# Kernel optimization log

Hardware: AMD Instinct MI355X
Metric: run time of the kernel (lower is better)

Reference implementation:

```python
import jax, jax.numpy as jnp
import numpy as np

DMODEL = 1024
DK = 64
DHEAD = 16
DEPTH = DK * DHEAD
N, LQ, L = 4, 4096, 4096
FAC1 = 1.0 / np.sqrt(DK)  # relu kernel scale folded into omega, as in reset()
EPS = 1e-6


def setup_inputs() -> dict:
    key = jax.random.key(0)
    ks = jax.random.split(key, 10)
    x = jax.random.normal(ks[0], (N, LQ, DMODEL), jnp.float32)
    y = jax.random.normal(ks[1], (N, L, DMODEL), jnp.float32)
    s_in = 1.0 / np.sqrt(DMODEL)
    s_depth = 1.0 / np.sqrt(DEPTH)
    # Linear weights stored as (in, out) so application is x @ W + b
    WQ = jax.random.normal(ks[2], (DMODEL, DEPTH), jnp.float32) * s_in
    WK = jax.random.normal(ks[3], (DMODEL, DEPTH), jnp.float32) * s_in
    WV = jax.random.normal(ks[4], (DMODEL, DEPTH), jnp.float32) * s_in
    WO = jax.random.normal(ks[5], (DEPTH, DMODEL), jnp.float32) * s_depth
    bQ = jnp.zeros((DEPTH,), jnp.float32)
    bK = jnp.zeros((DEPTH,), jnp.float32)
    bV = jnp.zeros((DEPTH,), jnp.float32)
    bO = jnp.zeros((DMODEL,), jnp.float32)
    # orthogonal random-feature projection: QR of gaussian, scaled by sqrt(dk), then *fac1 (relu)
    g = np.random.default_rng(0).standard_normal((DK, DK)).astype(np.float32)
    qmat, _ = np.linalg.qr(g)
    omega = jnp.asarray(qmat * np.sqrt(DK) * FAC1, dtype=jnp.float32)
    return dict(x=x, y=y, WQ=WQ, bQ=bQ, WK=WK, bK=bK, WV=WV, bV=bV,
                WO=WO, bO=bO, omega=omega)


def reference(x, y, WQ, bQ, WK, bK, WV, bV, WO, bO, omega):
    n, lq, _ = x.shape
    l = y.shape[1]
    # project and split heads: (n, h, L, dk)
    q = (x @ WQ + bQ).reshape(n, lq, DHEAD, DK).transpose(0, 2, 1, 3)
    k = (y @ WK + bK).reshape(n, l, DHEAD, DK).transpose(0, 2, 1, 3)
    v = (y @ WV + bV).reshape(n, l, DHEAD, DK).transpose(0, 2, 1, 3)
    # relu random-feature map phi(x) = relu(x @ omega) + eps
    q = jax.nn.relu(q @ omega) + EPS
    k = jax.nn.relu(k @ omega) + EPS
    # linear attention: out = phi(q) @ (phi(k)^T @ v) / (phi(q) @ phi(k)^T @ 1)
    kv = jnp.einsum('nhld,nhle->nhde', k, v)          # (n, h, dk, dk)
    ksum = jnp.sum(k, axis=2)                          # (n, h, dk)
    d_inv = jnp.einsum('nhqd,nhd->nhq', q, ksum)[..., None]
    out = jnp.einsum('nhqd,nhde->nhqe', q, kv) / d_inv  # (n, h, Lq, dk)
    out = out.transpose(0, 2, 1, 3).reshape(n, lq, DEPTH)
    return out @ WO + bO
```

## Files before the change

### kernel.cpp

```cpp
#include <hip/hip_runtime.h>

#define EPSF 1e-6f

typedef _Float16 f16x8 __attribute__((ext_vector_type(8)));
typedef _Float16 f16x4 __attribute__((ext_vector_type(4)));
typedef float    f32x4 __attribute__((ext_vector_type(4)));

#define GLL16(gp, lp) __builtin_amdgcn_global_load_lds( \
    (const __attribute__((address_space(1))) void*)(gp), \
    (__attribute__((address_space(3))) void*)(lp), 16, 0, 0)

__global__ __launch_bounds__(256) void cvt_f16(const float* __restrict__ in,
                                               _Float16* __restrict__ out, int n8) {
    int idx = blockIdx.x * 256 + threadIdx.x;
    int stride = gridDim.x * 256;
    for (; idx < n8; idx += stride) {
        const float4* p = (const float4*)in + (size_t)idx * 2;
        float4 a = p[0], b = p[1];
        f16x8 o;
        o[0] = (_Float16)a.x; o[1] = (_Float16)a.y; o[2] = (_Float16)a.z; o[3] = (_Float16)a.w;
        o[4] = (_Float16)b.x; o[5] = (_Float16)b.y; o[6] = (_Float16)b.z; o[7] = (_Float16)b.w;
        *(f16x8*)(out + (size_t)idx * 8) = o;
    }
}

__global__ __launch_bounds__(256) void build_obdT(const float* __restrict__ omega,
                                                  _Float16* __restrict__ obdT) {
    int idx = blockIdx.x * 256 + threadIdx.x;
    int c = idx >> 10, k = idx & 1023;
    float v = ((c >> 6) == (k >> 6)) ? omega[(k & 63) * 64 + (c & 63)] : 0.f;
    obdT[idx] = (_Float16)v;
}

__global__ __launch_bounds__(256) void transpose_cvt(const float* __restrict__ in,
                                                     _Float16* __restrict__ out) {
    __shared__ float tile[64][65];
    const int t = threadIdx.x;
    const int k0 = blockIdx.x * 64, n0 = blockIdx.y * 64;
#pragma unroll
    for (int j = 0; j < 16; j++) {
        int idx = j * 256 + t; int r = idx >> 6, c = idx & 63;
        tile[r][c] = in[(size_t)(k0 + r) * 1024 + n0 + c];
    }
    __syncthreads();
#pragma unroll
    for (int j = 0; j < 16; j++) {
        int idx = j * 256 + t; int rn = idx >> 6, ck = idx & 63;
        out[(size_t)(n0 + rn) * 1024 + k0 + ck] = (_Float16)tile[ck][rn];
    }
}

__global__ __launch_bounds__(256) void prep_bias(const float* __restrict__ bQ,
                                                 const float* __restrict__ bK,
                                                 const float* __restrict__ bV,
                                                 const float* __restrict__ omega,
                                                 float* __restrict__ bQf,
                                                 float* __restrict__ bkv) {
    int c = blockIdx.x * 256 + threadIdx.x;
    int h = c >> 6, e = c & 63;
    float sq = 0.f, sk = 0.f;
    for (int d = 0; d < 64; d++) {
        float o = omega[d * 64 + e];
        sq += bQ[h * 64 + d] * o;
        sk += bK[h * 64 + d] * o;
    }
    bQf[c] = sq;
    bkv[c] = sk;
    bkv[1024 + c] = bV[c];
}

__global__ __launch_bounds__(256) void gemm_fold(const _Float16* __restrict__ A,
                                                 const _Float16* __restrict__ Bt,
                                                 _Float16* __restrict__ out0,
                                                 _Float16* __restrict__ out1) {
    const int K = 1024;
    __shared__ __align__(16) _Float16 Asm[128 * 32];
    __shared__ __align__(16) _Float16 Bsm[128 * 32];
    const int t = threadIdx.x, lane = t & 63, w = t >> 6;
    const int bm = blockIdx.y * 128, bn = blockIdx.x * 128;
    const int wm = (w >> 1) * 64, wn = (w & 1) * 64;
    const int r15 = lane & 15, slog = lane >> 4;

    int aoff[4], boff[4];
#pragma unroll
    for (int m = 0; m < 4; m++) {
        int ra = wm + m * 16 + r15;
        aoff[m] = ra * 32 + (slog ^ ((ra >> 1) & 3)) * 8;
        int rb = wn + m * 16 + r15;
        boff[m] = rb * 32 + (slog ^ ((rb >> 1) & 3)) * 8;
    }
    f32x4 acc[4][4];
#pragma unroll
    for (int m = 0; m < 4; m++)
#pragma unroll
        for (int n = 0; n < 4; n++) acc[m][n] = (f32x4){0.f, 0.f, 0.f, 0.f};

    for (int kt = 0; kt < K; kt += 32) {
        __syncthreads();
#pragma unroll
        for (int i = 0; i < 2; i++) {
            int seg = i * 256 + w * 64 + lane;
            int r = seg >> 2, sp = seg & 3;
            int sg = sp ^ ((r >> 1) & 3);
            GLL16(A  + (size_t)(bm + r) * K + kt + sg * 8, Asm + (size_t)(i * 256 + w * 64) * 8);
            GLL16(Bt + (size_t)(bn + r) * K + kt + sg * 8, Bsm + (size_t)(i * 256 + w * 64) * 8);
        }
        __syncthreads();
        f16x8 av[4], bv[4];
#pragma unroll
        for (int m = 0; m < 4; m++) av[m] = *(const f16x8*)(Asm + aoff[m]);
#pragma unroll
        for (int n = 0; n < 4; n++) bv[n] = *(const f16x8*)(Bsm + boff[n]);
#pragma unroll
        for (int m = 0; m < 4; m++)
#pragma unroll
            for (int n = 0; n < 4; n++)
                acc[m][n] = __builtin_amdgcn_mfma_f32_16x16x32_f16(av[m], bv[n], acc[m][n], 0, 0, 0);
    }

#pragma unroll
    for (int m = 0; m < 4; m++) {
        int row0 = bm + wm + m * 16 + slog * 4;
        _Float16* C = (row0 < 1024) ? out0 : out1;
        int l = row0 & 1023;
#pragma unroll
        for (int n = 0; n < 4; n++) {
            int colg = bn + wn + n * 16 + r15;
            f16x4 p;
#pragma unroll
            for (int j = 0; j < 4; j++) p[j] = (_Float16)acc[m][n][j];
            *(f16x4*)(C + (size_t)colg * 1024 + l) = p;
        }
    }
}

template<int EPI>
__global__ __launch_bounds__(512, 2) void gemm256(const _Float16* __restrict__ A,
                                                  const _Float16* __restrict__ Bt,
                                                  const float* __restrict__ bias,
                                                  void* __restrict__ out0,
                                                  void* __restrict__ out1,
                                                  int M, int N, int K, int nbn) {
    __shared__ __align__(16) char lds[131072];
    const int t = threadIdx.x, lane = t & 63, w = t >> 6;
    const int nwg = gridDim.x;
    const int f = (blockIdx.x & 7) * (nwg >> 3) + (blockIdx.x >> 3);
    const int bm = (f / nbn) * 256, bn = (f % nbn) * 256;
    const int wm = (w & 1) * 128, wn = (w >> 1) * 64;
    const int r15 = lane & 15, hi = lane >> 4;
    const int srow = lane >> 2, sp = lane & 3;

    int aoff[8], boff[4];
#pragma unroll
    for (int m = 0; m < 8; m++) {
        int r = wm + m * 16 + r15;
        aoff[m] = r * 64 + (((hi + (r >> 1)) & 3) << 4);
    }
#pragma unroll
    for (int n = 0; n < 4; n++) {
        int r = wn + n * 16 + r15;
        boff[n] = r * 64 + (((hi + (r >> 1)) & 3) << 4);
    }

    f32x4 acc[8][4];
#pragma unroll
    for (int m = 0; m < 8; m++)
#pragma unroll
        for (int n = 0; n < 4; n++) acc[m][n] = (f32x4){0.f, 0.f, 0.f, 0.f};

    auto stage = [&](int s) {
        char* base = lds + (s & 3) * 32768;
        int kt = s * 32;
#pragma unroll
        for (int p = 0; p < 2; p++) {
            int row = w * 32 + p * 16 + srow;
            int sg = (sp - ((row >> 1) & 3)) & 3;
            GLL16(A  + (size_t)(bm + row) * K + kt + sg * 8, base + w * 2048 + p * 1024);
            GLL16(Bt + (size_t)(bn + row) * K + kt + sg * 8, base + 16384 + w * 2048 + p * 1024);
        }
    };

    const int NS = K >> 5;
    stage(0); stage(1); stage(2);
    asm volatile("s_waitcnt vmcnt(8)" ::: "memory");
    asm volatile("s_barrier" ::: "memory");
    for (int s = 0; s < NS; ++s) {
        const char* La = lds + (s & 3) * 32768;
        const char* Lb = La + 16384;
        if (s + 3 < NS) stage(s + 3);
        f16x8 bv[4], avL[4];
#pragma unroll
        for (int n = 0; n < 4; n++) bv[n] = *(const f16x8*)(Lb + boff[n]);
#pragma unroll
        for (int m = 0; m < 4; m++) avL[m] = *(const f16x8*)(La + aoff[m]);
        asm volatile("s_barrier" ::: "memory");
        asm volatile("s_waitcnt lgkmcnt(0)" ::: "memory");
        __builtin_amdgcn_s_setprio(1);
#pragma unroll
        for (int m = 0; m < 4; m++)
#pragma unroll
            for (int n = 0; n < 4; n++)
                acc[m][n] = __builtin_amdgcn_mfma_f32_16x16x32_f16(avL[m], bv[n], acc[m][n], 0, 0, 0);
        __builtin_amdgcn_s_setprio(0);
        asm volatile("s_barrier" ::: "memory");
        f16x8 avH[4];
#pragma unroll
        for (int m = 0; m < 4; m++) avH[m] = *(const f16x8*)(La + aoff[m + 4]);
        if (s + 3 < NS)      asm volatile("s_waitcnt vmcnt(8)" ::: "memory");
        else if (s + 2 < NS) asm volatile("s_waitcnt vmcnt(4)" ::: "memory");
        else                 asm volatile("s_waitcnt vmcnt(0)" ::: "memory");
        asm volatile("s_barrier" ::: "memory");
        asm volatile("s_waitcnt lgkmcnt(0)" ::: "memory");
        __builtin_amdgcn_s_setprio(1);
#pragma unroll
        for (int m = 0; m < 4; m++)
#pragma unroll
            for (int n = 0; n < 4; n++)
                acc[m + 4][n] = __builtin_amdgcn_mfma_f32_16x16x32_f16(avH[m], bv[n], acc[m + 4][n], 0, 0, 0);
        __builtin_amdgcn_s_setprio(0);
        asm volatile("s_barrier" ::: "memory");
    }

    if (EPI == 3) {
        char* LW = lds + w * 16384;
        const int colg0 = bn + wn;
        const bool isK = colg0 < 1024;
        _Float16* Cb = isK ? (_Float16*)out0 : (_Float16*)out1;
        const int hd = (isK ? colg0 : colg0 - 1024) >> 6;
        const int nb = bm >> 12;
        const int l0 = (bm & 4095) + wm;
#pragma unroll
        for (int m = 0; m < 8; m++)
#pragma unroll
            for (int n = 0; n < 4; n++) {
                int d = n * 16 + r15;
                float bs = bias[colg0 + d];
                f16x4 pk;
#pragma unroll
                for (int j = 0; j < 4; j++) {
                    float xv = acc[m][n][j] + bs;
                    if (isK) xv = fmaxf(xv, 0.f) + EPSF;
                    pk[j] = (_Float16)xv;
                }
                *(f16x4*)(LW + d * 256 + ((m * 32 + hi * 8) ^ ((d & 15) << 4))) = pk;
            }
        _Float16* basep = Cb + (size_t)(nb * 16 + hd) * 64 * 4096 + l0;
#pragma unroll
        for (int pass = 0; pass < 16; pass++) {
            int d = pass * 4 + hi;
            f16x8 v = *(const f16x8*)(LW + d * 256 + ((r15 * 16) ^ ((d & 15) << 4)));
            *(f16x8*)(basep + (size_t)d * 4096 + r15 * 8) = v;
        }
    } else {
#pragma unroll
        for (int m = 0; m < 8; m++) {
            int row0 = bm + wm + m * 16 + hi * 4;
#pragma unroll
            for (int n = 0; n < 4; n++) {
                int colg = bn + wn + n * 16 + r15;
                float bs = bias ? bias[colg] : 0.f;
#pragma unroll
                for (int j = 0; j < 4; j++) {
                    float xv = acc[m][n][j] + bs;
                    if (EPI == 1) {
                        xv = fmaxf(xv, 0.f) + EPSF;
                        ((_Float16*)out0)[(size_t)(row0 + j) * N + colg] = (_Float16)xv;
                    } else {
                        ((float*)out0)[(size_t)(row0 + j) * N + colg] = xv;
                    }
                }
            }
        }
    }
}

__global__ __launch_bounds__(256) void ksum_kernel(const _Float16* __restrict__ KphiT,
                                                   float* __restrict__ ksum) {
    const int t = threadIdx.x, lane = t & 63, w = t >> 6;
    const int gid = blockIdx.x;
    const int head = gid >> 4;
    const int d = (gid & 15) * 4 + w;
    const _Float16* src = KphiT + ((size_t)head * 64 + d) * 4096;
    float s = 0.f;
#pragma unroll
    for (int i = 0; i < 8; i++) {
        f16x8 v = *(const f16x8*)(src + (size_t)(i * 64 + lane) * 8);
#pragma unroll
        for (int j = 0; j < 8; j++) s += (float)v[j];
    }
#pragma unroll
    for (int o = 32; o; o >>= 1) s += __shfl_xor(s, o, 64);
    if (lane == 0) ksum[(size_t)head * 64 + d] = s;
}

__global__ __launch_bounds__(256) void kvt_kernel(const _Float16* __restrict__ Vt,
                                                  const _Float16* __restrict__ KphiT,
                                                  float* __restrict__ kvpart) {
    const int t = threadIdx.x, lane = t & 63, w = t >> 6;
    const int head = blockIdx.y;
    const int l0 = blockIdx.x * 1024;
    __shared__ __align__(16) _Float16 As[64 * 128];
    __shared__ __align__(16) _Float16 Bs[64 * 128];
    const int r15 = lane & 15, slog = lane >> 4;
    f32x4 acc[4][4];
#pragma unroll
    for (int m = 0; m < 4; m++)
#pragma unroll
        for (int n = 0; n < 4; n++) acc[m][n] = (f32x4){0.f, 0.f, 0.f, 0.f};

    for (int it = 0; it < 8; it++) {
        __syncthreads();
        int lbase = l0 + it * 128;
#pragma unroll
        for (int i = 0; i < 4; i++) {
            int seg = i * 256 + w * 64 + lane;
            int r = seg >> 4, sp2 = seg & 15;
            int sg = sp2 ^ (r & 15);
            GLL16(Vt    + ((size_t)head * 64 + r) * 4096 + lbase + sg * 8, As + (size_t)(i * 256 + w * 64) * 8);
            GLL16(KphiT + ((size_t)head * 64 + r) * 4096 + lbase + sg * 8, Bs + (size_t)(i * 256 + w * 64) * 8);
        }
        __syncthreads();
        f16x8 av[4], bv[4];
#pragma unroll
        for (int m = 0; m < 4; m++) {
            int r = m * 16 + r15;
            int s2 = w * 4 + slog;
            int ph = s2 ^ (r & 15);
            av[m] = *(const f16x8*)(As + r * 128 + ph * 8);
            bv[m] = *(const f16x8*)(Bs + r * 128 + ph * 8);
        }
#pragma unroll
        for (int m = 0; m < 4; m++)
#pragma unroll
            for (int n = 0; n < 4; n++)
                acc[m][n] = __builtin_amdgcn_mfma_f32_16x16x32_f16(av[m], bv[n], acc[m][n], 0, 0, 0);
    }
    float* red = (float*)As;
    for (int ww = 0; ww < 4; ww++) {
        __syncthreads();
        if (w == ww) {
#pragma unroll
            for (int m = 0; m < 4; m++)
#pragma unroll
                for (int n = 0; n < 4; n++)
#pragma unroll
                    for (int j = 0; j < 4; j++) {
                        int row = m * 16 + slog * 4 + j, col = n * 16 + r15;
                        if (ww == 0) red[row * 64 + col] = acc[m][n][j];
                        else         red[row * 64 + col] += acc[m][n][j];
                    }
        }
    }
    __syncthreads();
    float* outp = kvpart + ((size_t)head * 4 + blockIdx.x) * 4096;
#pragma unroll
    for (int i = 0; i < 16; i++) { int idx = i * 256 + t; outp[idx] = red[idx]; }
}

__global__ __launch_bounds__(256) void numdiv_kernel(const _Float16* __restrict__ Qphi,
                                                     const float* __restrict__ kvpart,
                                                     const float* __restrict__ ksum,
                                                     _Float16* __restrict__ U) {
    const int t = threadIdx.x, lane = t & 63, w = t >> 6;
    const int h = blockIdx.y;
    const int m0 = blockIdx.x * 256;
    const int nb = m0 >> 12;
    const int head = nb * 16 + h;
    __shared__ __align__(16) _Float16 Qs[256 * 64];
    __shared__ __align__(16) _Float16 Bs[64 * 64];
    __shared__ float ksl[64];

#pragma unroll
    for (int i = 0; i < 8; i++) {
        int seg = i * 256 + w * 64 + lane;
        int r = seg >> 3, sp = seg & 7;
        int sg = sp ^ (r & 7);
        GLL16(Qphi + (size_t)(m0 + r) * 1024 + h * 64 + sg * 8, Qs + (size_t)(i * 256 + w * 64) * 8);
    }
#pragma unroll
    for (int i = 0; i < 2; i++) {
        int sidx = i * 256 + t;
        int r = sidx >> 3, p = sidx & 7;
        int sg = p ^ (r & 7);
        const float* s0 = kvpart + (size_t)head * 4 * 4096 + r * 64 + sg * 8;
        float4 v0 = {0.f, 0.f, 0.f, 0.f}, v1 = {0.f, 0.f, 0.f, 0.f};
#pragma unroll
        for (int c = 0; c < 4; c++) {
            float4 a = *(const float4*)(s0 + c * 4096);
            float4 b = *(const float4*)(s0 + c * 4096 + 4);
            v0.x += a.x; v0.y += a.y; v0.z += a.z; v0.w += a.w;
            v1.x += b.x; v1.y += b.y; v1.z += b.z; v1.w += b.w;
        }
        f16x8 o;
        o[0] = (_Float16)v0.x; o[1] = (_Float16)v0.y; o[2] = (_Float16)v0.z; o[3] = (_Float16)v0.w;
        o[4] = (_Float16)v1.x; o[5] = (_Float16)v1.y; o[6] = (_Float16)v1.z; o[7] = (_Float16)v1.w;
        *(f16x8*)(Bs + sidx * 8) = o;
    }
    if (t < 64) ksl[t] = ksum[(size_t)head * 64 + t];
    __syncthreads();

    const int r15 = lane & 15, slog = lane >> 4;
    f32x4 acc[4][4];
#pragma unroll
    for (int m = 0; m < 4; m++)
#pragma unroll
        for (int n = 0; n < 4; n++) acc[m][n] = (f32x4){0.f, 0.f, 0.f, 0.f};
    float dp[4] = {0.f, 0.f, 0.f, 0.f};

#pragma unroll
    for (int kk = 0; kk < 2; kk++) {
        float ks[8];
#pragma unroll
        for (int j = 0; j < 8; j++) ks[j] = ksl[kk * 32 + slog * 8 + j];
        f16x8 av[4], bv[4];
#pragma unroll
        for (int m = 0; m < 4; m++) {
            int r = w * 64 + m * 16 + r15;
            int ph = (kk * 4 + slog) ^ (r & 7);
            av[m] = *(const f16x8*)(Qs + r * 64 + ph * 8);
        }
#pragma unroll
        for (int n = 0; n < 4; n++) {
            int r = n * 16 + r15;
            int ph = (kk * 4 + slog) ^ (r & 7);
            bv[n] = *(const f16x8*)(Bs + r * 64 + ph * 8);
        }
#pragma unroll
        for (int m = 0; m < 4; m++)
#pragma unroll
            for (int j = 0; j < 8; j++) dp[m] += (float)av[m][j] * ks[j];
#pragma unroll
        for (int m = 0; m < 4; m++)
#pragma unroll
            for (int n = 0; n < 4; n++)
                acc[m][n] = __builtin_amdgcn_mfma_f32_16x16x32_f16(av[m], bv[n], acc[m][n], 0, 0, 0);
    }
#pragma unroll
    for (int m = 0; m < 4; m++) {
        dp[m] += __shfl_xor(dp[m], 16, 64);
        dp[m] += __shfl_xor(dp[m], 32, 64);
    }
#pragma unroll
    for (int m = 0; m < 4; m++) {
#pragma unroll
        for (int j = 0; j < 4; j++) {
            float den = __shfl(dp[m], slog * 4 + j, 64);
            float inv = __builtin_amdgcn_rcpf(den);
            int row = m0 + w * 64 + m * 16 + slog * 4 + j;
#pragma unroll
            for (int n = 0; n < 4; n++)
                U[(size_t)row * 1024 + h * 64 + n * 16 + r15] = (_Float16)(acc[m][n][j] * inv);
        }
    }
}

extern "C" void kernel_launch(void* const* d_in, const int* in_sizes, int n_in,
                              void* d_out, int out_size, void* d_ws, size_t ws_size,
                              hipStream_t stream) {
    (void)in_sizes; (void)n_in; (void)out_size; (void)ws_size;
    const float* x     = (const float*)d_in[0];
    const float* y     = (const float*)d_in[1];
    const float* WQ    = (const float*)d_in[2];
    const float* bQ    = (const float*)d_in[3];
    const float* WK    = (const float*)d_in[4];
    const float* bK    = (const float*)d_in[5];
    const float* WV    = (const float*)d_in[6];
    const float* bV    = (const float*)d_in[7];
    const float* WO    = (const float*)d_in[8];
    const float* bO    = (const float*)d_in[9];
    const float* omega = (const float*)d_in[10];

    char* ws = (char*)d_ws;
    size_t off = 0;
    auto alloc = [&](size_t bytes) { void* p = ws + off; off += (bytes + 255) & ~(size_t)255; return p; };
    const size_t BIG = (size_t)16384 * 1024 * 2;
    _Float16* xb    = (_Float16*)alloc(BIG);
    _Float16* yb    = (_Float16*)alloc(BIG);
    _Float16* WQKb  = (_Float16*)alloc((size_t)2048 * 1024 * 2);
    _Float16* obdT  = (_Float16*)alloc(1024 * 1024 * 2);
    _Float16* Wqt   = (_Float16*)alloc(1024 * 1024 * 2);
    _Float16* Wkvt  = (_Float16*)alloc((size_t)2048 * 1024 * 2);
    _Float16* Wot   = (_Float16*)alloc(1024 * 1024 * 2);
    float*    bQf   = (float*)alloc(1024 * 4);
    float*    bkv   = (float*)alloc(2048 * 4);
    _Float16* Qphi  = (_Float16*)alloc(BIG);
    _Float16* KphiT = (_Float16*)alloc(BIG);
    _Float16* Vt    = (_Float16*)alloc(BIG);
    float*    kvpart= (float*)alloc((size_t)256 * 4096 * 4);
    float*    ksum  = (float*)alloc((size_t)64 * 64 * 4);
    _Float16* U     = xb;

    cvt_f16<<<2048, 256, 0, stream>>>(x, xb, 16384 * 1024 / 8);
    cvt_f16<<<2048, 256, 0, stream>>>(y, yb, 16384 * 1024 / 8);
    cvt_f16<<<512, 256, 0, stream>>>(WQ, WQKb, 1024 * 1024 / 8);
    cvt_f16<<<512, 256, 0, stream>>>(WK, WQKb + (size_t)1024 * 1024, 1024 * 1024 / 8);
    build_obdT<<<4096, 256, 0, stream>>>(omega, obdT);
    transpose_cvt<<<dim3(16, 16), 256, 0, stream>>>(WV, Wkvt + (size_t)1024 * 1024);
    transpose_cvt<<<dim3(16, 16), 256, 0, stream>>>(WO, Wot);
    prep_bias<<<4, 256, 0, stream>>>(bQ, bK, bV, omega, bQf, bkv);
    gemm_fold<<<dim3(8, 16), 256, 0, stream>>>(WQKb, obdT, Wqt, Wkvt);
    gemm256<1><<<256, 512, 0, stream>>>(xb, Wqt, bQf, Qphi, nullptr, 16384, 1024, 1024, 4);
    gemm256<3><<<512, 512, 0, stream>>>(yb, Wkvt, bkv, KphiT, Vt, 16384, 2048, 1024, 8);
    ksum_kernel<<<1024, 256, 0, stream>>>(KphiT, ksum);
    kvt_kernel<<<dim3(4, 64), 256, 0, stream>>>(Vt, KphiT, kvpart);
    numdiv_kernel<<<dim3(64, 16), 256, 0, stream>>>(Qphi, kvpart, ksum, U);
    gemm256<2><<<256, 512, 0, stream>>>(U, Wot, bO, d_out, nullptr, 16384, 1024, 1024, 4);
}
```

Measured before the change: 288.0 us.

## Switch gemm256 to 32x32x16 MFMA with single-barrier pipeline and merge prep kernels

The main 256x256 GEMM now uses 32x32x16 f16 MFMA tiles instead of 16x16x32. Each wave does 4x2 fragments over two k-substeps, and the epilogues are remapped to the new accumulator layout. The K loop is reduced from several barriers per stage to one wait plus barrier at the top. The small prep launches are also merged: x/y conversion, WQ/WK conversion, and omega block-diagonal plus bias folding each become one kernel. This is meant to cut LDS reads and barrier stalls per MFMA and to remove launch overhead. It risks LDS bank conflicts with the new swizzle mapping, higher register pressure, and less latency hiding.

```diff
diff --git a/kernel.cpp b/kernel.cpp
--- a/kernel.cpp
+++ b/kernel.cpp
@@ -5,31 +5,50 @@
 typedef _Float16 f16x8 __attribute__((ext_vector_type(8)));
 typedef _Float16 f16x4 __attribute__((ext_vector_type(4)));
 typedef float    f32x4 __attribute__((ext_vector_type(4)));
+typedef float    f32x16 __attribute__((ext_vector_type(16)));
 
 #define GLL16(gp, lp) __builtin_amdgcn_global_load_lds( \
     (const __attribute__((address_space(1))) void*)(gp), \
     (__attribute__((address_space(3))) void*)(lp), 16, 0, 0)
 
-__global__ __launch_bounds__(256) void cvt_f16(const float* __restrict__ in,
-                                               _Float16* __restrict__ out, int n8) {
+__global__ __launch_bounds__(256) void cvt2_f16(const float* __restrict__ inA,
+                                                _Float16* __restrict__ outA,
+                                                const float* __restrict__ inB,
+                                                _Float16* __restrict__ outB, int n8each) {
     int idx = blockIdx.x * 256 + threadIdx.x;
-    int stride = gridDim.x * 256;
-    for (; idx < n8; idx += stride) {
-        const float4* p = (const float4*)in + (size_t)idx * 2;
-        float4 a = p[0], b = p[1];
-        f16x8 o;
-        o[0] = (_Float16)a.x; o[1] = (_Float16)a.y; o[2] = (_Float16)a.z; o[3] = (_Float16)a.w;
-        o[4] = (_Float16)b.x; o[5] = (_Float16)b.y; o[6] = (_Float16)b.z; o[7] = (_Float16)b.w;
-        *(f16x8*)(out + (size_t)idx * 8) = o;
-    }
-}
-
-__global__ __launch_bounds__(256) void build_obdT(const float* __restrict__ omega,
-                                                  _Float16* __restrict__ obdT) {
+    const float* in = inA; _Float16* out = outA;
+    if (idx >= n8each) { idx -= n8each; in = inB; out = outB; }
+    const float4* p = (const float4*)in + (size_t)idx * 2;
+    float4 a = p[0], b = p[1];
+    f16x8 o;
+    o[0] = (_Float16)a.x; o[1] = (_Float16)a.y; o[2] = (_Float16)a.z; o[3] = (_Float16)a.w;
+    o[4] = (_Float16)b.x; o[5] = (_Float16)b.y; o[6] = (_Float16)b.z; o[7] = (_Float16)b.w;
+    *(f16x8*)(out + (size_t)idx * 8) = o;
+}
+
+__global__ __launch_bounds__(256) void prep_all(const float* __restrict__ omega,
+                                                const float* __restrict__ bQ,
+                                                const float* __restrict__ bK,
+                                                const float* __restrict__ bV,
+                                                _Float16* __restrict__ obdT,
+                                                float* __restrict__ bQf,
+                                                float* __restrict__ bkv) {
     int idx = blockIdx.x * 256 + threadIdx.x;
     int c = idx >> 10, k = idx & 1023;
     float v = ((c >> 6) == (k >> 6)) ? omega[(k & 63) * 64 + (c & 63)] : 0.f;
     obdT[idx] = (_Float16)v;
+    if (idx < 1024) {
+        int h = idx >> 6, e = idx & 63;
+        float sq = 0.f, sk = 0.f;
+        for (int d = 0; d < 64; d++) {
+            float o = omega[d * 64 + e];
+            sq += bQ[h * 64 + d] * o;
+            sk += bK[h * 64 + d] * o;
+        }
+        bQf[idx] = sq;
+        bkv[idx] = sk;
+        bkv[1024 + idx] = bV[idx];
+    }
 }
 
 __global__ __launch_bounds__(256) void transpose_cvt(const float* __restrict__ in,
@@ -48,25 +67,6 @@
         int idx = j * 256 + t; int rn = idx >> 6, ck = idx & 63;
         out[(size_t)(n0 + rn) * 1024 + k0 + ck] = (_Float16)tile[ck][rn];
     }
-}
-
-__global__ __launch_bounds__(256) void prep_bias(const float* __restrict__ bQ,
-                                                 const float* __restrict__ bK,
-                                                 const float* __restrict__ bV,
-                                                 const float* __restrict__ omega,
-                                                 float* __restrict__ bQf,
-                                                 float* __restrict__ bkv) {
-    int c = blockIdx.x * 256 + threadIdx.x;
-    int h = c >> 6, e = c & 63;
-    float sq = 0.f, sk = 0.f;
-    for (int d = 0; d < 64; d++) {
-        float o = omega[d * 64 + e];
-        sq += bQ[h * 64 + d] * o;
-        sk += bK[h * 64 + d] * o;
-    }
-    bQf[c] = sq;
-    bkv[c] = sk;
-    bkv[1024 + c] = bV[c];
 }
 
 __global__ __launch_bounds__(256) void gemm_fold(const _Float16* __restrict__ A,
@@ -147,26 +147,33 @@
     const int f = (blockIdx.x & 7) * (nwg >> 3) + (blockIdx.x >> 3);
     const int bm = (f / nbn) * 256, bn = (f % nbn) * 256;
     const int wm = (w & 1) * 128, wn = (w >> 1) * 64;
-    const int r15 = lane & 15, hi = lane >> 4;
+    const int l31 = lane & 31, hi2 = lane >> 5;
+    const int r15 = lane & 15, hi4 = lane >> 4;
     const int srow = lane >> 2, sp = lane & 3;
 
-    int aoff[8], boff[4];
-#pragma unroll
-    for (int m = 0; m < 8; m++) {
-        int r = wm + m * 16 + r15;
-        aoff[m] = r * 64 + (((hi + (r >> 1)) & 3) << 4);
-    }
-#pragma unroll
-    for (int n = 0; n < 4; n++) {
-        int r = wn + n * 16 + r15;
-        boff[n] = r * 64 + (((hi + (r >> 1)) & 3) << 4);
-    }
-
-    f32x4 acc[8][4];
-#pragma unroll
-    for (int m = 0; m < 8; m++)
-#pragma unroll
-        for (int n = 0; n < 4; n++) acc[m][n] = (f32x4){0.f, 0.f, 0.f, 0.f};
+    int aoff[4][2], boff[2][2];
+#pragma unroll
+    for (int mf = 0; mf < 4; mf++) {
+        int r = wm + mf * 32 + l31;
+#pragma unroll
+        for (int ks = 0; ks < 2; ks++)
+            aoff[mf][ks] = r * 64 + (((ks * 2 + hi2 + (r >> 1)) & 3) << 4);
+    }
+#pragma unroll
+    for (int nf = 0; nf < 2; nf++) {
+        int r = wn + nf * 32 + l31;
+#pragma unroll
+        for (int ks = 0; ks < 2; ks++)
+            boff[nf][ks] = r * 64 + (((ks * 2 + hi2 + (r >> 1)) & 3) << 4);
+    }
+
+    f32x16 acc[4][2];
+#pragma unroll
+    for (int mf = 0; mf < 4; mf++)
+#pragma unroll
+        for (int nf = 0; nf < 2; nf++)
+#pragma unroll
+            for (int j = 0; j < 16; j++) acc[mf][nf][j] = 0.f;
 
     auto stage = [&](int s) {
         char* base = lds + (s & 3) * 32768;
@@ -182,46 +189,36 @@
 
     const int NS = K >> 5;
     stage(0); stage(1); stage(2);
-    asm volatile("s_waitcnt vmcnt(8)" ::: "memory");
-    asm volatile("s_barrier" ::: "memory");
     for (int s = 0; s < NS; ++s) {
+        if (s + 2 < NS)      asm volatile("s_waitcnt vmcnt(8)" ::: "memory");
+        else if (s + 1 < NS) asm volatile("s_waitcnt vmcnt(4)" ::: "memory");
+        else                 asm volatile("s_waitcnt vmcnt(0)" ::: "memory");
+        asm volatile("s_barrier" ::: "memory");
+        if (s + 3 < NS) stage(s + 3);
         const char* La = lds + (s & 3) * 32768;
         const char* Lb = La + 16384;
-        if (s + 3 < NS) stage(s + 3);
-        f16x8 bv[4], avL[4];
-#pragma unroll
-        for (int n = 0; n < 4; n++) bv[n] = *(const f16x8*)(Lb + boff[n]);
-#pragma unroll
-        for (int m = 0; m < 4; m++) avL[m] = *(const f16x8*)(La + aoff[m]);
+        f16x8 bv[2][2], av[4][2];
+#pragma unroll
+        for (int nf = 0; nf < 2; nf++)
+#pragma unroll
+            for (int ks = 0; ks < 2; ks++) bv[nf][ks] = *(const f16x8*)(Lb + boff[nf][ks]);
+#pragma unroll
+        for (int mf = 0; mf < 4; mf++)
+#pragma unroll
+            for (int ks = 0; ks < 2; ks++) av[mf][ks] = *(const f16x8*)(La + aoff[mf][ks]);
+        __builtin_amdgcn_s_setprio(1);
+#pragma unroll
+        for (int mf = 0; mf < 4; mf++)
+#pragma unroll
+            for (int nf = 0; nf < 2; nf++)
+#pragma unroll
+                for (int ks = 0; ks < 2; ks++)
+                    acc[mf][nf] = __builtin_amdgcn_mfma_f32_32x32x16_f16(av[mf][ks], bv[nf][ks], acc[mf][nf], 0, 0, 0);
+        __builtin_amdgcn_s_setprio(0);
+    }
+
+    if (EPI == 3) {
         asm volatile("s_barrier" ::: "memory");
-        asm volatile("s_waitcnt lgkmcnt(0)" ::: "memory");
-        __builtin_amdgcn_s_setprio(1);
-#pragma unroll
-        for (int m = 0; m < 4; m++)
-#pragma unroll
-            for (int n = 0; n < 4; n++)
-                acc[m][n] = __builtin_amdgcn_mfma_f32_16x16x32_f16(avL[m], bv[n], acc[m][n], 0, 0, 0);
-        __builtin_amdgcn_s_setprio(0);
-        asm volatile("s_barrier" ::: "memory");
-        f16x8 avH[4];
-#pragma unroll
-        for (int m = 0; m < 4; m++) avH[m] = *(const f16x8*)(La + aoff[m + 4]);
-        if (s + 3 < NS)      asm volatile("s_waitcnt vmcnt(8)" ::: "memory");
-        else if (s + 2 < NS) asm volatile("s_waitcnt vmcnt(4)" ::: "memory");
-        else                 asm volatile("s_waitcnt vmcnt(0)" ::: "memory");
-        asm volatile("s_barrier" ::: "memory");
-        asm volatile("s_waitcnt lgkmcnt(0)" ::: "memory");
-        __builtin_amdgcn_s_setprio(1);
-#pragma unroll
-        for (int m = 0; m < 4; m++)
-#pragma unroll
-            for (int n = 0; n < 4; n++)
-                acc[m + 4][n] = __builtin_amdgcn_mfma_f32_16x16x32_f16(avH[m], bv[n], acc[m + 4][n], 0, 0, 0);
-        __builtin_amdgcn_s_setprio(0);
-        asm volatile("s_barrier" ::: "memory");
-    }
-
-    if (EPI == 3) {
         char* LW = lds + w * 16384;
         const int colg0 = bn + wn;
         const bool isK = colg0 < 1024;
@@ -230,47 +227,53 @@
         const int nb = bm >> 12;
         const int l0 = (bm & 4095) + wm;
 #pragma unroll
-        for (int m = 0; m < 8; m++)
-#pragma unroll
-            for (int n = 0; n < 4; n++) {
-                int d = n * 16 + r15;
-                float bs = bias[colg0 + d];
-                f16x4 pk;
-#pragma unroll
-                for (int j = 0; j < 4; j++) {
-                    float xv = acc[m][n][j] + bs;
-                    if (isK) xv = fmaxf(xv, 0.f) + EPSF;
-                    pk[j] = (_Float16)xv;
+        for (int mf = 0; mf < 4; mf++)
+#pragma unroll
+            for (int nf = 0; nf < 2; nf++) {
+                int dl = nf * 32 + l31;
+                float bs = bias[colg0 + dl];
+#pragma unroll
+                for (int g = 0; g < 4; g++) {
+                    f16x4 pk;
+#pragma unroll
+                    for (int j = 0; j < 4; j++) {
+                        float xv = acc[mf][nf][g * 4 + j] + bs;
+                        if (isK) xv = fmaxf(xv, 0.f) + EPSF;
+                        pk[j] = (_Float16)xv;
+                    }
+                    int lby = mf * 64 + g * 16 + hi2 * 8;
+                    *(f16x4*)(LW + dl * 256 + (lby ^ ((dl & 15) << 4))) = pk;
                 }
-                *(f16x4*)(LW + d * 256 + ((m * 32 + hi * 8) ^ ((d & 15) << 4))) = pk;
             }
         _Float16* basep = Cb + (size_t)(nb * 16 + hd) * 64 * 4096 + l0;
 #pragma unroll
         for (int pass = 0; pass < 16; pass++) {
-            int d = pass * 4 + hi;
+            int d = pass * 4 + hi4;
             f16x8 v = *(const f16x8*)(LW + d * 256 + ((r15 * 16) ^ ((d & 15) << 4)));
             *(f16x8*)(basep + (size_t)d * 4096 + r15 * 8) = v;
         }
     } else {
 #pragma unroll
-        for (int m = 0; m < 8; m++) {
-            int row0 = bm + wm + m * 16 + hi * 4;
-#pragma unroll
-            for (int n = 0; n < 4; n++) {
-                int colg = bn + wn + n * 16 + r15;
+        for (int mf = 0; mf < 4; mf++)
+#pragma unroll
+            for (int nf = 0; nf < 2; nf++) {
+                int colg = bn + wn + nf * 32 + l31;
                 float bs = bias ? bias[colg] : 0.f;
 #pragma unroll
-                for (int j = 0; j < 4; j++) {
-                    float xv = acc[m][n][j] + bs;
-                    if (EPI == 1) {
-                        xv = fmaxf(xv, 0.f) + EPSF;
-                        ((_Float16*)out0)[(size_t)(row0 + j) * N + colg] = (_Float16)xv;
-                    } else {
-                        ((float*)out0)[(size_t)(row0 + j) * N + colg] = xv;
+                for (int g = 0; g < 4; g++) {
+                    int row0 = bm + wm + mf * 32 + 8 * g + 4 * hi2;
+#pragma unroll
+                    for (int j = 0; j < 4; j++) {
+                        float xv = acc[mf][nf][g * 4 + j] + bs;
+                        if (EPI == 1) {
+                            xv = fmaxf(xv, 0.f) + EPSF;
+                            ((_Float16*)out0)[(size_t)(row0 + j) * N + colg] = (_Float16)xv;
+                        } else {
+                            ((float*)out0)[(size_t)(row0 + j) * N + colg] = xv;
+                        }
                     }
                 }
             }
-        }
     }
 }
 
@@ -490,14 +493,11 @@
     float*    ksum  = (float*)alloc((size_t)64 * 64 * 4);
     _Float16* U     = xb;
 
-    cvt_f16<<<2048, 256, 0, stream>>>(x, xb, 16384 * 1024 / 8);
-    cvt_f16<<<2048, 256, 0, stream>>>(y, yb, 16384 * 1024 / 8);
-    cvt_f16<<<512, 256, 0, stream>>>(WQ, WQKb, 1024 * 1024 / 8);
-    cvt_f16<<<512, 256, 0, stream>>>(WK, WQKb + (size_t)1024 * 1024, 1024 * 1024 / 8);
-    build_obdT<<<4096, 256, 0, stream>>>(omega, obdT);
+    cvt2_f16<<<16384, 256, 0, stream>>>(x, xb, y, yb, 16384 * 1024 / 8);
+    cvt2_f16<<<1024, 256, 0, stream>>>(WQ, WQKb, WK, WQKb + (size_t)1024 * 1024, 1024 * 1024 / 8);
+    prep_all<<<4096, 256, 0, stream>>>(omega, bQ, bK, bV, obdT, bQf, bkv);
     transpose_cvt<<<dim3(16, 16), 256, 0, stream>>>(WV, Wkvt + (size_t)1024 * 1024);
     transpose_cvt<<<dim3(16, 16), 256, 0, stream>>>(WO, Wot);
-    prep_bias<<<4, 256, 0, stream>>>(bQ, bK, bV, omega, bQf, bkv);
     gemm_fold<<<dim3(8, 16), 256, 0, stream>>>(WQKb, obdT, Wqt, Wkvt);
     gemm256<1><<<256, 512, 0, stream>>>(xb, Wqt, bQf, Qphi, nullptr, 16384, 1024, 1024, 4);
     gemm256<3><<<512, 512, 0, stream>>>(yb, Wkvt, bkv, KphiT, Vt, 16384, 2048, 1024, 8);
```

Result: no change. 287.5 us (-0.2%).
